# Performance work log

Hardware: AMD Instinct MI355X
Metric: run time of the kernel (lower is better)

Reference implementation:

```python
import jax, jax.numpy as jnp
import numpy as np
from jax import lax

L, E, H, V, T = 4096, 512, 512, 50000, 32
START, END = 0, 1
NEG = -10000.0


def setup_inputs() -> dict:
    key = jax.random.key(0)
    ks = jax.random.split(key, 16)
    s = 0.1  # keep activations in a sane range
    inp = {
        'sentence': jax.random.randint(ks[0], (L,), 0, V, dtype=jnp.int32),
        'embed':  jax.random.normal(ks[1], (V, E)) * s,
        'w_ih_f': jax.random.normal(ks[2], (4 * H, E)) * s,
        'w_hh_f': jax.random.normal(ks[3], (4 * H, H)) * s,
        'b_ih_f': jax.random.normal(ks[4], (4 * H,)) * s,
        'b_hh_f': jax.random.normal(ks[5], (4 * H,)) * s,
        'w_ih_b': jax.random.normal(ks[6], (4 * H, E)) * s,
        'w_hh_b': jax.random.normal(ks[7], (4 * H, H)) * s,
        'b_ih_b': jax.random.normal(ks[8], (4 * H,)) * s,
        'b_hh_b': jax.random.normal(ks[9], (4 * H,)) * s,
        'w_out':  jax.random.normal(ks[10], (T, 2 * H)) * s,
        'b_out':  jax.random.normal(ks[11], (T,)) * s,
        'h0':     jax.random.normal(ks[13], (2, H)),
        'c0':     jax.random.normal(ks[14], (2, H)),
    }
    trans = jax.random.normal(ks[12], (T, T))
    # CRF constraints: never transition into START, never leave from END
    trans = trans.at[START, :].set(NEG).at[:, END].set(NEG)
    inp['trans'] = trans
    return inp


def _lstm_dir(xs, w_ih, w_hh, b_ih, b_hh, h0, c0, reverse):
    # xs: (L, E). PyTorch gate order: i, f, g, o. Precompute input projection.
    x_proj = xs @ w_ih.T + (b_ih + b_hh)  # (L, 4H)

    def step(carry, xp):
        h, c = carry
        gates = xp + h @ w_hh.T
        i, f, g, o = jnp.split(gates, 4)
        i, f, o = jax.nn.sigmoid(i), jax.nn.sigmoid(f), jax.nn.sigmoid(o)
        g = jnp.tanh(g)
        c = f * c + i * g
        h = o * jnp.tanh(c)
        return (h, c), h

    _, hs = lax.scan(step, (h0, c0), x_proj, reverse=reverse)
    return hs  # (L, H)


def reference(sentence, embed, w_ih_f, w_hh_f, b_ih_f, b_hh_f,
              w_ih_b, w_hh_b, b_ih_b, b_hh_b, w_out, b_out, trans, h0, c0):
    xs = embed[sentence]  # (L, E)
    hs_f = _lstm_dir(xs, w_ih_f, w_hh_f, b_ih_f, b_hh_f, h0[0], c0[0], False)
    hs_b = _lstm_dir(xs, w_ih_b, w_hh_b, b_ih_b, b_hh_b, h0[1], c0[1], True)
    feats = jnp.concatenate([hs_f, hs_b], axis=1) @ w_out.T + b_out  # (L, T)

    # Viterbi forward: trans[next, prev]
    init_v = jnp.full((T,), NEG).at[START].set(0.0)

    def vstep(fv, feat):
        scores = trans + fv[None, :]          # (T_next, T_prev)
        bptr = jnp.argmax(scores, axis=1)     # (T,)
        fv_new = jnp.max(scores, axis=1) + feat
        return fv_new, bptr

    fv, bptrs = lax.scan(vstep, init_v, feats)  # bptrs: (L, T)
    terminal = fv + trans[END]
    score = jnp.max(terminal)
    last_tag = jnp.argmax(terminal)

    # Backtrace (reverse scan): path[L-1]=last_tag, path[i]=bptrs[i+1][path[i+1]]
    def back(tag, bp):
        return bp[tag], tag

    _, path = lax.scan(back, last_tag, bptrs, reverse=True)  # (L,)
    return score, path
```

## Files before the change

### kernel.cpp

```cpp
#include <hip/hip_runtime.h>
#include <stdint.h>

#define L_SEQ 4096
#define E_DIM 512
#define H_DIM 512
#define G_DIM 2048
#define NTAG  32

typedef unsigned long long u64;
typedef unsigned short     u16;
typedef unsigned char      u8;

__device__ __forceinline__ float bf2f(u16 u) {
    union { unsigned int i; float f; } v; v.i = ((unsigned int)u) << 16; return v.f;
}
__device__ __forceinline__ bool sniff_f32(const void* trans_raw) {
    const u16* p = (const u16*)trans_raw;
    return p[0] != p[1];
}
__device__ __forceinline__ float ldf(const void* base, long idx, bool isf32) {
    if (isf32) return ((const float*)base)[idx];
    return bf2f(((const u16*)base)[idx]);
}
__device__ __forceinline__ void unpack8_bf16(const u16* src, float* dst) {
    uint4 p = *(const uint4*)src;
    dst[0] = __uint_as_float(p.x << 16); dst[1] = __uint_as_float(p.x & 0xffff0000u);
    dst[2] = __uint_as_float(p.y << 16); dst[3] = __uint_as_float(p.y & 0xffff0000u);
    dst[4] = __uint_as_float(p.z << 16); dst[5] = __uint_as_float(p.z & 0xffff0000u);
    dst[6] = __uint_as_float(p.w << 16); dst[7] = __uint_as_float(p.w & 0xffff0000u);
}

#define LOG2E 1.44269504088896340736f
__device__ __forceinline__ float fsig(float x) {
    return __builtin_amdgcn_rcpf(1.f + __builtin_amdgcn_exp2f(-x * LOG2E));
}
__device__ __forceinline__ float ftanh(float x) {
    return 1.f - 2.f * __builtin_amdgcn_rcpf(1.f + __builtin_amdgcn_exp2f(x * (2.f * LOG2E)));
}

__global__ __launch_bounds__(256) void k_xproj(
    const int* __restrict__ sent, const void* __restrict__ embed,
    const void* __restrict__ w_ih_f, const void* __restrict__ b_ih_f, const void* __restrict__ b_hh_f,
    const void* __restrict__ w_ih_b, const void* __restrict__ b_ih_b, const void* __restrict__ b_hh_b,
    const void* __restrict__ trans_raw,
    float* __restrict__ xp_f, float* __restrict__ xp_b)
{
    const bool isf32 = sniff_f32(trans_raw);
    const int dir = (int)blockIdx.y;
    const void* W  = dir ? w_ih_b : w_ih_f;
    const void* bi = dir ? b_ih_b : b_ih_f;
    const void* bh = dir ? b_hh_b : b_hh_f;
    float* xp = dir ? xp_b : xp_f;
    const int m0 = (int)blockIdx.x * 16;
    const int tid = (int)threadIdx.x;

    __shared__ float xs[16][520];
    __shared__ float wl[16][520];

    {
        const int r = tid >> 4, c0 = (tid & 15) * 32;
        const long row = sent[m0 + r];
        if (isf32) {
            const float* src = (const float*)embed + row * E_DIM + c0;
            #pragma unroll
            for (int i = 0; i < 32; i += 4) *(float4*)&xs[r][c0 + i] = *(const float4*)(src + i);
        } else {
            const u16* src = (const u16*)embed + row * E_DIM + c0;
            #pragma unroll
            for (int i = 0; i < 32; i += 8) unpack8_bf16(src + i, &xs[r][c0 + i]);
        }
    }
    __syncthreads();

    const int mi = tid >> 4, gi = tid & 15;
    for (int gb = 0; gb < 128; ++gb) {
        const int g0 = gb * 16;
        {
            const int r = tid >> 4, c0 = (tid & 15) * 32;
            if (isf32) {
                const float* src = (const float*)W + (long)(g0 + r) * E_DIM + c0;
                #pragma unroll
                for (int i = 0; i < 32; i += 4) *(float4*)&wl[r][c0 + i] = *(const float4*)(src + i);
            } else {
                const u16* src = (const u16*)W + (long)(g0 + r) * E_DIM + c0;
                #pragma unroll
                for (int i = 0; i < 32; i += 8) unpack8_bf16(src + i, &wl[r][c0 + i]);
            }
        }
        __syncthreads();

        float acc = 0.f;
        #pragma unroll 4
        for (int k = 0; k < E_DIM; k += 4) {
            const float4 xv = *(const float4*)&xs[mi][k];
            const float4 wv = *(const float4*)&wl[gi][k];
            acc = fmaf(xv.x, wv.x, acc); acc = fmaf(xv.y, wv.y, acc);
            acc = fmaf(xv.z, wv.z, acc); acc = fmaf(xv.w, wv.w, acc);
        }
        const int g = g0 + gi;
        const float bias = ldf(bi, g, isf32) + ldf(bh, g, isf32);
        xp[(long)(m0 + mi) * G_DIM + g] = acc + bias;
        __syncthreads();
    }
}

__global__ __launch_bounds__(256, 1) void k_lstm(
    const void* __restrict__ w_hh_f, const void* __restrict__ w_hh_b,
    const void* __restrict__ h0, const void* __restrict__ c0,
    const void* __restrict__ trans_raw,
    const float* __restrict__ xp_f, const float* __restrict__ xp_b,
    u64* __restrict__ hsT_f, u64* __restrict__ hsT_b)
{
    const bool isf32 = sniff_f32(trans_raw);
    const int dir = (int)(blockIdx.x >> 5);
    const int wg  = (int)(blockIdx.x & 31);
    const int j0  = wg * 16;
    const void* Whh = dir ? w_hh_b : w_hh_f;
    const float* xp = dir ? xp_b : xp_f;
    u64* hsT        = dir ? hsT_b : hsT_f;

    const int tid = (int)threadIdx.x;
    const int rp  = tid >> 3;
    const int ks  = tid & 7;
    const int d   = rp >> 1;
    const int gp  = rp & 1;
    const int g0r = gp * 2;

    __shared__ float h_lds[512 + 32];

    float wreg[2][64];
    #pragma unroll
    for (int rl = 0; rl < 2; ++rl) {
        const long roff = (long)((g0r + rl) * H_DIM + j0 + d) * H_DIM + ks * 64;
        if (isf32) {
            const float* wrow = (const float*)Whh + roff;
            #pragma unroll
            for (int b = 0; b < 16; ++b) *(float4*)&wreg[rl][b * 4] = *(const float4*)(wrow + b * 4);
        } else {
            const u16* wrow = (const u16*)Whh + roff;
            #pragma unroll
            for (int b = 0; b < 8; ++b) unpack8_bf16(wrow + b * 8, &wreg[rl][b * 8]);
        }
    }

    {
        const int w0 = tid * 2;
        h_lds[w0 + ((w0 >> 6) << 2)]     = ldf(h0, dir * H_DIM + w0, isf32);
        h_lds[w0 + 1 + ((w0 >> 6) << 2)] = ldf(h0, dir * H_DIM + w0 + 1, isf32);
    }

    const bool is_act = ((tid & 15) == 0);
    const int  jown   = j0 + d;
    float cst = 0.f;
    if (is_act) cst = ldf(c0, dir * H_DIM + jown, isf32);

    const int b16 = tid >> 4, off = tid & 15;
    const int pidx = is_act ? -1 : (b16 * 15 + off - 1);
    int jw0 = 0, jw1 = 0, jw2 = -1;
    if (pidx >= 0) {
        const int w0 = 2 * pidx, w1 = 2 * pidx + 1;
        jw0 = w0 + (w0 >= j0 ? 16 : 0);
        jw1 = w1 + (w1 >= j0 ? 16 : 0);
        if (pidx < 16) { const int w2 = 480 + pidx; jw2 = w2 + (w2 >= j0 ? 16 : 0); }
    }

    int t = dir ? (L_SEQ - 1) : 0;
    float xc0 = 0, xc1 = 0, xc2 = 0, xc3 = 0, xn0 = 0, xn1 = 0, xn2 = 0, xn3 = 0;
    if (is_act) {
        const float* xr = xp + (long)t * G_DIM + jown;
        xn0 = xr[0]; xn1 = xr[H_DIM]; xn2 = xr[2 * H_DIM]; xn3 = xr[3 * H_DIM];
    }
    __syncthreads();

    #pragma unroll 1
    for (int k = 0; k < L_SEQ; ++k) {
        t = dir ? (L_SEQ - 1 - k) : k;
        if (is_act) {
            xc0 = xn0; xc1 = xn1; xc2 = xn2; xc3 = xn3;
            if (k + 1 < L_SEQ) {
                const int nt = dir ? (t - 1) : (t + 1);
                const float* xr = xp + (long)nt * G_DIM + jown;
                xn0 = xr[0]; xn1 = xr[H_DIM]; xn2 = xr[2 * H_DIM]; xn3 = xr[3 * H_DIM];
            }
        }

        float a0 = 0, a1 = 0;
        const float4* hb = (const float4*)(h_lds + ks * 68);
        #pragma unroll
        for (int q = 0; q < 16; ++q) {
            const float4 hv = hb[q];
            a0 = fmaf(wreg[0][4*q+0], hv.x, a0); a0 = fmaf(wreg[0][4*q+1], hv.y, a0);
            a0 = fmaf(wreg[0][4*q+2], hv.z, a0); a0 = fmaf(wreg[0][4*q+3], hv.w, a0);
            a1 = fmaf(wreg[1][4*q+0], hv.x, a1); a1 = fmaf(wreg[1][4*q+1], hv.y, a1);
            a1 = fmaf(wreg[1][4*q+2], hv.z, a1); a1 = fmaf(wreg[1][4*q+3], hv.w, a1);
        }
        #pragma unroll
        for (int m = 1; m < 8; m <<= 1) { a0 += __shfl_xor(a0, m); a1 += __shfl_xor(a1, m); }
        const float b0 = __shfl_xor(a0, 8);
        const float b1 = __shfl_xor(a1, 8);

        if (is_act) {
            const float iv = fsig(a0 + xc0);
            const float fo = fsig(a1 + xc1);
            const float gv = ftanh(b0 + xc2);
            const float ov = fsig(b1 + xc3);
            cst = fo * cst + iv * gv;
            const float hv2 = ov * ftanh(cst);
            h_lds[jown + ((jown >> 6) << 2)] = hv2;
            const u64 pk = (((u64)(unsigned)(k + 1)) << 32) | (u64)__float_as_uint(hv2);
            __hip_atomic_store(&hsT[(long)t * H_DIM + jown], pk,
                               __ATOMIC_RELAXED, __HIP_MEMORY_SCOPE_AGENT);
        }

        if (k + 1 < L_SEQ && pidx >= 0) {
            const unsigned tagv = (unsigned)(k + 1);
            u64* pa0 = &hsT[(long)t * H_DIM + jw0];
            u64* pa1 = &hsT[(long)t * H_DIM + jw1];
            u64* pa2 = (jw2 >= 0) ? &hsT[(long)t * H_DIM + jw2] : pa0;
            u64 v0 = 0, v1 = 0, v2 = 0;
            bool q0 = false, q1 = false, q2 = (jw2 < 0);
            do {
                if (!q0) { v0 = __hip_atomic_load(pa0, __ATOMIC_RELAXED, __HIP_MEMORY_SCOPE_AGENT); }
                if (!q1) { v1 = __hip_atomic_load(pa1, __ATOMIC_RELAXED, __HIP_MEMORY_SCOPE_AGENT); }
                if (!q2) { v2 = __hip_atomic_load(pa2, __ATOMIC_RELAXED, __HIP_MEMORY_SCOPE_AGENT); }
                q0 = q0 || ((unsigned)(v0 >> 32) == tagv);
                q1 = q1 || ((unsigned)(v1 >> 32) == tagv);
                q2 = q2 || ((unsigned)(v2 >> 32) == tagv);
            } while (!(q0 && q1 && q2));
            h_lds[jw0 + ((jw0 >> 6) << 2)] = __uint_as_float((unsigned)v0);
            h_lds[jw1 + ((jw1 >> 6) << 2)] = __uint_as_float((unsigned)v1);
            if (jw2 >= 0) h_lds[jw2 + ((jw2 >> 6) << 2)] = __uint_as_float((unsigned)v2);
        }
        __syncthreads();
    }
}

__global__ __launch_bounds__(256) void k_feats(
    const u64* __restrict__ hsT_f, const u64* __restrict__ hsT_b,
    const void* __restrict__ w_out, const void* __restrict__ b_out,
    const void* __restrict__ trans_raw, float* __restrict__ feats)
{
    const bool isf32 = sniff_f32(trans_raw);
    const int n  = (int)threadIdx.x & 31;
    const int tl = (int)threadIdx.x >> 5;
    const int t  = (int)blockIdx.x * 8 + tl;
    const float* hf  = (const float*)(hsT_f + (long)t * H_DIM);
    const float* hbp = (const float*)(hsT_b + (long)t * H_DIM);
    float acc = ldf(b_out, n, isf32);
    if (isf32) {
        const float* wf = (const float*)w_out + (long)n * 1024;
        const float* wb = wf + 512;
        #pragma unroll 4
        for (int j2 = 0; j2 < 256; ++j2) {
            acc = fmaf(hf [4 * j2],     wf[2 * j2],     acc);
            acc = fmaf(hf [4 * j2 + 2], wf[2 * j2 + 1], acc);
            acc = fmaf(hbp[4 * j2],     wb[2 * j2],     acc);
            acc = fmaf(hbp[4 * j2 + 2], wb[2 * j2 + 1], acc);
        }
    } else {
        const unsigned int* wf = (const unsigned int*)((const u16*)w_out + (long)n * 1024);
        const unsigned int* wb = (const unsigned int*)((const u16*)w_out + (long)n * 1024 + 512);
        #pragma unroll 4
        for (int j2 = 0; j2 < 256; ++j2) {
            const unsigned int wp = wf[j2];
            const unsigned int wq = wb[j2];
            acc = fmaf(hf [4 * j2],     __uint_as_float(wp << 16),         acc);
            acc = fmaf(hf [4 * j2 + 2], __uint_as_float(wp & 0xffff0000u), acc);
            acc = fmaf(hbp[4 * j2],     __uint_as_float(wq << 16),         acc);
            acc = fmaf(hbp[4 * j2 + 2], __uint_as_float(wq & 0xffff0000u), acc);
        }
    }
    feats[(long)t * 32 + n] = acc;
}

__global__ __launch_bounds__(64) void k_viterbi(
    const float* __restrict__ feats, const void* __restrict__ trans_raw,
    u8* __restrict__ bptr, float* __restrict__ out)
{
    const bool isf32 = sniff_f32(trans_raw);
    const int lane = (int)threadIdx.x;
    const int n = lane & 31, half = lane >> 5;
    __shared__ u8 mlds[64 * 32];
    __shared__ u8 entry[64];

    float tr[16];
    #pragma unroll
    for (int i = 0; i < 16; ++i) tr[i] = ldf(trans_raw, n * 32 + half * 16 + i, isf32);
    const float tr_end = ldf(trans_raw, 32 + n, isf32);

    float fvreg = (n == 0) ? 0.f : -10000.f;
    float fnext = feats[n];
    #pragma unroll 1
    for (int tt = 0; tt < L_SEQ; ++tt) {
        const float fcur = fnext;
        const int nt = (tt + 1 < L_SEQ) ? tt + 1 : tt;
        fnext = feats[(long)nt * 32 + n];

        float best = -3.4e38f; int bp = 0;
        #pragma unroll
        for (int i = 0; i < 16; ++i) {
            const float c = tr[i] + __shfl(fvreg, half * 16 + i);
            if (c > best) { best = c; bp = half * 16 + i; }
        }
        const float ob = __shfl_xor(best, 32);
        const int  obp = __shfl_xor(bp, 32);
        if (ob > best || (ob == best && obp < bp)) { best = ob; bp = obp; }

        fvreg = best + fcur;
        if (half == 0) bptr[(long)tt * 32 + n] = (u8)bp;
    }

    float term = (half == 0) ? (fvreg + tr_end) : -3.4e38f;
    int   ti   = (half == 0) ? n : 1000;
    #pragma unroll
    for (int m = 1; m < 64; m <<= 1) {
        const float ov = __shfl_xor(term, m);
        const int   oi = __shfl_xor(ti, m);
        if (ov > term || (ov == term && oi < ti)) { term = ov; ti = oi; }
    }
    if (lane == 0) out[0] = term;
    __syncthreads();

    unsigned cur[32];
    #pragma unroll
    for (int ch = 0; ch < 32; ++ch) cur[ch] = (unsigned)ch;
    const int cbase = lane * 64;
    for (int s = 63; s >= 0; --s) {
        const u8* row = bptr + (long)(cbase + s) * 32;
        #pragma unroll
        for (int ch = 0; ch < 32; ++ch) cur[ch] = row[cur[ch]];
    }
    #pragma unroll
    for (int ch = 0; ch < 32; ++ch) mlds[lane * 32 + ch] = (u8)cur[ch];
    __syncthreads();

    if (lane == 0) {
        int tag = ti;
        for (int c = 63; c >= 0; --c) { entry[c] = (u8)tag; tag = mlds[c * 32 + tag]; }
    }
    __syncthreads();

    {
        int tag = entry[lane];
        for (int s = 63; s >= 0; --s) {
            const int gidx = cbase + s;
            out[1 + gidx] = (float)tag;
            tag = bptr[(long)gidx * 32 + tag];
        }
    }
}

extern "C" void kernel_launch(void* const* d_in, const int* in_sizes, int n_in,
                              void* d_out, int out_size, void* d_ws, size_t ws_size,
                              hipStream_t stream)
{
    (void)in_sizes; (void)n_in; (void)out_size; (void)ws_size;
    const int* sent  = (const int*)d_in[0];
    const void* embed  = d_in[1];
    const void* w_ih_f = d_in[2];
    const void* w_hh_f = d_in[3];
    const void* b_ih_f = d_in[4];
    const void* b_hh_f = d_in[5];
    const void* w_ih_b = d_in[6];
    const void* w_hh_b = d_in[7];
    const void* b_ih_b = d_in[8];
    const void* b_hh_b = d_in[9];
    const void* w_out  = d_in[10];
    const void* b_out  = d_in[11];
    const void* h0     = d_in[12];
    const void* c0     = d_in[13];
    const void* trans  = d_in[14];

    char* ws = (char*)d_ws;
    float* xp_f  = (float*)(ws);
    float* xp_b  = (float*)(ws + (32ull << 20));
    u64*   hsT_f = (u64*)(ws + (64ull << 20));
    u64*   hsT_b = (u64*)(ws + (80ull << 20));
    float* feats = (float*)(ws);
    u8*    bptr  = (u8*)(ws + (1ull << 20));

    k_xproj<<<dim3(256, 2), 256, 0, stream>>>(sent, embed,
        w_ih_f, b_ih_f, b_hh_f, w_ih_b, b_ih_b, b_hh_b, trans, xp_f, xp_b);
    k_lstm<<<64, 256, 0, stream>>>(w_hh_f, w_hh_b, h0, c0, trans, xp_f, xp_b, hsT_f, hsT_b);
    k_feats<<<512, 256, 0, stream>>>(hsT_f, hsT_b, w_out, b_out, trans, feats);
    k_viterbi<<<1, 64, 0, stream>>>(feats, trans, bptr, (float*)d_out);
}
```

Before: 12.61 ms.

## Pin each LSTM direction's workgroups to one XCD and exchange h via small ring

The LSTM kernel now launches 2048 blocks. Each block reads its XCC_ID and claims a slot through atomics so that all 32 workgroups of a direction sit on the same XCD; surplus blocks exit. Per-step hidden-state exchange moves from a full-sequence tagged array to a 4-slot ring with salted tags, polled first with workgroup-scope CAS (aiming for L2-local hits) and falling back to agent-scope loads. Hidden states are also written to a plain float array, which lets the feats kernel use vectorized loads. This risks a deadlock or wrong ordering if the placement assumptions fail, and adds launch overhead from the excess blocks.

```diff
diff --git a/kernel.cpp b/kernel.cpp
--- a/kernel.cpp
+++ b/kernel.cpp
@@ -6,6 +6,7 @@
 #define H_DIM 512
 #define G_DIM 2048
 #define NTAG  32
+#define RING_SLOTS 4
 
 typedef unsigned long long u64;
 typedef unsigned short     u16;
@@ -38,13 +39,27 @@
     return 1.f - 2.f * __builtin_amdgcn_rcpf(1.f + __builtin_amdgcn_exp2f(x * (2.f * LOG2E)));
 }
 
+__device__ __forceinline__ int get_xcc_id() {
+    unsigned x;
+    asm volatile("s_getreg_b32 %0, hwreg(HW_REG_XCC_ID)" : "=s"(x));
+    return (int)(x & 0xf);
+}
+
 __global__ __launch_bounds__(256) void k_xproj(
     const int* __restrict__ sent, const void* __restrict__ embed,
     const void* __restrict__ w_ih_f, const void* __restrict__ b_ih_f, const void* __restrict__ b_hh_f,
     const void* __restrict__ w_ih_b, const void* __restrict__ b_ih_b, const void* __restrict__ b_hh_b,
     const void* __restrict__ trans_raw,
-    float* __restrict__ xp_f, float* __restrict__ xp_b)
+    float* __restrict__ xp_f, float* __restrict__ xp_b,
+    int* __restrict__ ctrl)
 {
+    if (blockIdx.x == 0 && blockIdx.y == 0 && threadIdx.x == 0) {
+        ctrl[0] = -1;
+        ctrl[1] = -1;
+        ctrl[2] = 0;
+        ctrl[3] = 0;
+        ctrl[4] = ctrl[4] + 8192;
+    }
     const bool isf32 = sniff_f32(trans_raw);
     const int dir = (int)blockIdx.y;
     const void* W  = dir ? w_ih_b : w_ih_f;
@@ -109,15 +124,44 @@
     const void* __restrict__ h0, const void* __restrict__ c0,
     const void* __restrict__ trans_raw,
     const float* __restrict__ xp_f, const float* __restrict__ xp_b,
-    u64* __restrict__ hsT_f, u64* __restrict__ hsT_b)
+    float* __restrict__ hs_f, float* __restrict__ hs_b,
+    u64* __restrict__ ring_f, u64* __restrict__ ring_b,
+    int* __restrict__ ctrl)
 {
+    __shared__ int   s_team[3];
+    __shared__ float h_lds[512 + 32];
+
+    if (threadIdx.x == 0) {
+        const int xcd = get_xcc_id();
+        int dir = -1, slot = -1;
+        int x0 = atomicCAS(&ctrl[0], -1, xcd);
+        if (x0 == -1) x0 = xcd;
+        if (x0 == xcd) {
+            slot = atomicAdd(&ctrl[2], 1);
+            if (slot < 32) dir = 0;
+        }
+        if (dir < 0) {
+            int x1 = atomicCAS(&ctrl[1], -1, xcd);
+            if (x1 == -1) x1 = xcd;
+            if (x1 == xcd) {
+                slot = atomicAdd(&ctrl[3], 1);
+                if (slot < 32) dir = 1;
+            }
+        }
+        s_team[0] = dir; s_team[1] = slot; s_team[2] = ctrl[4];
+    }
+    __syncthreads();
+    const int dir = s_team[0];
+    const int wg  = s_team[1];
+    const unsigned salt = (unsigned)s_team[2];
+    if (dir < 0) return;
+
     const bool isf32 = sniff_f32(trans_raw);
-    const int dir = (int)(blockIdx.x >> 5);
-    const int wg  = (int)(blockIdx.x & 31);
     const int j0  = wg * 16;
     const void* Whh = dir ? w_hh_b : w_hh_f;
     const float* xp = dir ? xp_b : xp_f;
-    u64* hsT        = dir ? hsT_b : hsT_f;
+    float* hs       = dir ? hs_b : hs_f;
+    u64* ring       = dir ? ring_b : ring_f;
 
     const int tid = (int)threadIdx.x;
     const int rp  = tid >> 3;
@@ -125,8 +169,6 @@
     const int d   = rp >> 1;
     const int gp  = rp & 1;
     const int g0r = gp * 2;
-
-    __shared__ float h_lds[512 + 32];
 
     float wreg[2][64];
     #pragma unroll
@@ -163,6 +205,7 @@
         jw1 = w1 + (w1 >= j0 ? 16 : 0);
         if (pidx < 16) { const int w2 = 480 + pidx; jw2 = w2 + (w2 >= j0 ? 16 : 0); }
     }
+    int slowmode = 0;
 
     int t = dir ? (L_SEQ - 1) : 0;
     float xc0 = 0, xc1 = 0, xc2 = 0, xc3 = 0, xn0 = 0, xn1 = 0, xn2 = 0, xn3 = 0;
@@ -175,6 +218,9 @@
     #pragma unroll 1
     for (int k = 0; k < L_SEQ; ++k) {
         t = dir ? (L_SEQ - 1 - k) : k;
+        const long rb = (long)(k & (RING_SLOTS - 1)) * H_DIM;
+        const unsigned tagv = salt + (unsigned)(k + 1);
+
         if (is_act) {
             xc0 = xn0; xc1 = xn1; xc2 = xn2; xc3 = xn3;
             if (k + 1 < L_SEQ) {
@@ -207,26 +253,42 @@
             cst = fo * cst + iv * gv;
             const float hv2 = ov * ftanh(cst);
             h_lds[jown + ((jown >> 6) << 2)] = hv2;
-            const u64 pk = (((u64)(unsigned)(k + 1)) << 32) | (u64)__float_as_uint(hv2);
-            __hip_atomic_store(&hsT[(long)t * H_DIM + jown], pk,
+            hs[(long)t * H_DIM + jown] = hv2;
+            const u64 pk = (((u64)tagv) << 32) | (u64)__float_as_uint(hv2);
+            __hip_atomic_store(&ring[rb + jown], pk,
                                __ATOMIC_RELAXED, __HIP_MEMORY_SCOPE_AGENT);
         }
 
         if (k + 1 < L_SEQ && pidx >= 0) {
-            const unsigned tagv = (unsigned)(k + 1);
-            u64* pa0 = &hsT[(long)t * H_DIM + jw0];
-            u64* pa1 = &hsT[(long)t * H_DIM + jw1];
-            u64* pa2 = (jw2 >= 0) ? &hsT[(long)t * H_DIM + jw2] : pa0;
+            u64* pa0 = &ring[rb + jw0];
+            u64* pa1 = &ring[rb + jw1];
+            u64* pa2 = (jw2 >= 0) ? &ring[rb + jw2] : pa0;
             u64 v0 = 0, v1 = 0, v2 = 0;
             bool q0 = false, q1 = false, q2 = (jw2 < 0);
-            do {
-                if (!q0) { v0 = __hip_atomic_load(pa0, __ATOMIC_RELAXED, __HIP_MEMORY_SCOPE_AGENT); }
-                if (!q1) { v1 = __hip_atomic_load(pa1, __ATOMIC_RELAXED, __HIP_MEMORY_SCOPE_AGENT); }
-                if (!q2) { v2 = __hip_atomic_load(pa2, __ATOMIC_RELAXED, __HIP_MEMORY_SCOPE_AGENT); }
-                q0 = q0 || ((unsigned)(v0 >> 32) == tagv);
-                q1 = q1 || ((unsigned)(v1 >> 32) == tagv);
-                q2 = q2 || ((unsigned)(v2 >> 32) == tagv);
-            } while (!(q0 && q1 && q2));
+            if (!slowmode) {
+                int spins = 0;
+                do {
+                    if (!q0) { u64 e = 0; __hip_atomic_compare_exchange_strong(pa0, &e, (u64)0,
+                                 __ATOMIC_RELAXED, __ATOMIC_RELAXED, __HIP_MEMORY_SCOPE_WORKGROUP);
+                               if ((unsigned)(e >> 32) == tagv) { v0 = e; q0 = true; } }
+                    if (!q1) { u64 e = 0; __hip_atomic_compare_exchange_strong(pa1, &e, (u64)0,
+                                 __ATOMIC_RELAXED, __ATOMIC_RELAXED, __HIP_MEMORY_SCOPE_WORKGROUP);
+                               if ((unsigned)(e >> 32) == tagv) { v1 = e; q1 = true; } }
+                    if (!q2) { u64 e = 0; __hip_atomic_compare_exchange_strong(pa2, &e, (u64)0,
+                                 __ATOMIC_RELAXED, __ATOMIC_RELAXED, __HIP_MEMORY_SCOPE_WORKGROUP);
+                               if ((unsigned)(e >> 32) == tagv) { v2 = e; q2 = true; } }
+                    if (q0 && q1 && q2) break;
+                } while (++spins < 64);
+                if (!(q0 && q1 && q2)) slowmode = 1;
+            }
+            while (!(q0 && q1 && q2)) {
+                if (!q0) { u64 x = __hip_atomic_load(pa0, __ATOMIC_RELAXED, __HIP_MEMORY_SCOPE_AGENT);
+                           if ((unsigned)(x >> 32) == tagv) { v0 = x; q0 = true; } }
+                if (!q1) { u64 x = __hip_atomic_load(pa1, __ATOMIC_RELAXED, __HIP_MEMORY_SCOPE_AGENT);
+                           if ((unsigned)(x >> 32) == tagv) { v1 = x; q1 = true; } }
+                if (!q2) { u64 x = __hip_atomic_load(pa2, __ATOMIC_RELAXED, __HIP_MEMORY_SCOPE_AGENT);
+                           if ((unsigned)(x >> 32) == tagv) { v2 = x; q2 = true; } }
+            }
             h_lds[jw0 + ((jw0 >> 6) << 2)] = __uint_as_float((unsigned)v0);
             h_lds[jw1 + ((jw1 >> 6) << 2)] = __uint_as_float((unsigned)v1);
             if (jw2 >= 0) h_lds[jw2 + ((jw2 >> 6) << 2)] = __uint_as_float((unsigned)v2);
@@ -236,7 +298,7 @@
 }
 
 __global__ __launch_bounds__(256) void k_feats(
-    const u64* __restrict__ hsT_f, const u64* __restrict__ hsT_b,
+    const float* __restrict__ hs_f, const float* __restrict__ hs_b,
     const void* __restrict__ w_out, const void* __restrict__ b_out,
     const void* __restrict__ trans_raw, float* __restrict__ feats)
 {
@@ -244,30 +306,43 @@
     const int n  = (int)threadIdx.x & 31;
     const int tl = (int)threadIdx.x >> 5;
     const int t  = (int)blockIdx.x * 8 + tl;
-    const float* hf  = (const float*)(hsT_f + (long)t * H_DIM);
-    const float* hbp = (const float*)(hsT_b + (long)t * H_DIM);
+    const float* hf = hs_f + (long)t * H_DIM;
+    const float* hb = hs_b + (long)t * H_DIM;
     float acc = ldf(b_out, n, isf32);
     if (isf32) {
         const float* wf = (const float*)w_out + (long)n * 1024;
         const float* wb = wf + 512;
         #pragma unroll 4
-        for (int j2 = 0; j2 < 256; ++j2) {
-            acc = fmaf(hf [4 * j2],     wf[2 * j2],     acc);
-            acc = fmaf(hf [4 * j2 + 2], wf[2 * j2 + 1], acc);
-            acc = fmaf(hbp[4 * j2],     wb[2 * j2],     acc);
-            acc = fmaf(hbp[4 * j2 + 2], wb[2 * j2 + 1], acc);
+        for (int j = 0; j < 512; j += 4) {
+            const float4 hv = *(const float4*)&hf[j];
+            const float4 wv = *(const float4*)&wf[j];
+            acc = fmaf(hv.x, wv.x, acc); acc = fmaf(hv.y, wv.y, acc);
+            acc = fmaf(hv.z, wv.z, acc); acc = fmaf(hv.w, wv.w, acc);
+            const float4 hv2 = *(const float4*)&hb[j];
+            const float4 wv2 = *(const float4*)&wb[j];
+            acc = fmaf(hv2.x, wv2.x, acc); acc = fmaf(hv2.y, wv2.y, acc);
+            acc = fmaf(hv2.z, wv2.z, acc); acc = fmaf(hv2.w, wv2.w, acc);
         }
     } else {
-        const unsigned int* wf = (const unsigned int*)((const u16*)w_out + (long)n * 1024);
-        const unsigned int* wb = (const unsigned int*)((const u16*)w_out + (long)n * 1024 + 512);
-        #pragma unroll 4
-        for (int j2 = 0; j2 < 256; ++j2) {
-            const unsigned int wp = wf[j2];
-            const unsigned int wq = wb[j2];
-            acc = fmaf(hf [4 * j2],     __uint_as_float(wp << 16),         acc);
-            acc = fmaf(hf [4 * j2 + 2], __uint_as_float(wp & 0xffff0000u), acc);
-            acc = fmaf(hbp[4 * j2],     __uint_as_float(wq << 16),         acc);
-            acc = fmaf(hbp[4 * j2 + 2], __uint_as_float(wq & 0xffff0000u), acc);
+        const u16* wfh = (const u16*)w_out + (long)n * 1024;
+        const u16* wbh = wfh + 512;
+        #pragma unroll 2
+        for (int j = 0; j < 512; j += 8) {
+            float wt[8];
+            unpack8_bf16(&wfh[j], wt);
+            const float4 h0v = *(const float4*)&hf[j];
+            const float4 h1v = *(const float4*)&hf[j + 4];
+            acc = fmaf(h0v.x, wt[0], acc); acc = fmaf(h0v.y, wt[1], acc);
+            acc = fmaf(h0v.z, wt[2], acc); acc = fmaf(h0v.w, wt[3], acc);
+            acc = fmaf(h1v.x, wt[4], acc); acc = fmaf(h1v.y, wt[5], acc);
+            acc = fmaf(h1v.z, wt[6], acc); acc = fmaf(h1v.w, wt[7], acc);
+            unpack8_bf16(&wbh[j], wt);
+            const float4 h2v = *(const float4*)&hb[j];
+            const float4 h3v = *(const float4*)&hb[j + 4];
+            acc = fmaf(h2v.x, wt[0], acc); acc = fmaf(h2v.y, wt[1], acc);
+            acc = fmaf(h2v.z, wt[2], acc); acc = fmaf(h2v.w, wt[3], acc);
+            acc = fmaf(h3v.x, wt[4], acc); acc = fmaf(h3v.y, wt[5], acc);
+            acc = fmaf(h3v.z, wt[6], acc); acc = fmaf(h3v.w, wt[7], acc);
         }
     }
     feats[(long)t * 32 + n] = acc;
@@ -374,14 +449,18 @@
     char* ws = (char*)d_ws;
     float* xp_f  = (float*)(ws);
     float* xp_b  = (float*)(ws + (32ull << 20));
-    u64*   hsT_f = (u64*)(ws + (64ull << 20));
-    u64*   hsT_b = (u64*)(ws + (80ull << 20));
+    float* hs_f  = (float*)(ws + (64ull << 20));
+    float* hs_b  = (float*)(ws + (72ull << 20));
+    u64*   ring_f = (u64*)(ws + (80ull << 20));
+    u64*   ring_b = (u64*)(ws + (80ull << 20) + (64u << 10));
+    int*   ctrl   = (int*)(ws + (80ull << 20) + (128u << 10));
     float* feats = (float*)(ws);
     u8*    bptr  = (u8*)(ws + (1ull << 20));
 
     k_xproj<<<dim3(256, 2), 256, 0, stream>>>(sent, embed,
-        w_ih_f, b_ih_f, b_hh_f, w_ih_b, b_ih_b, b_hh_b, trans, xp_f, xp_b);
-    k_lstm<<<64, 256, 0, stream>>>(w_hh_f, w_hh_b, h0, c0, trans, xp_f, xp_b, hsT_f, hsT_b);
-    k_feats<<<512, 256, 0, stream>>>(hsT_f, hsT_b, w_out, b_out, trans, feats);
+        w_ih_f, b_ih_f, b_hh_f, w_ih_b, b_ih_b, b_hh_b, trans, xp_f, xp_b, ctrl);
+    k_lstm<<<2048, 256, 0, stream>>>(w_hh_f, w_hh_b, h0, c0, trans, xp_f, xp_b,
+                                     hs_f, hs_b, ring_f, ring_b, ctrl);
+    k_feats<<<512, 256, 0, stream>>>(hs_f, hs_b, w_out, b_out, trans, feats);
     k_viterbi<<<1, 64, 0, stream>>>(feats, trans, bptr, (float*)d_out);
 }
```

New measurement: 32.36 ms. +156.6%, slower.
